# Kernel optimization log

Measured on AMD Instinct MI355X. Metric: run time of the kernel, lower is better.

Reference implementation:

```python
import jax, jax.numpy as jnp
import numpy as np

EPS = 1e-5

def layer_norm(x, g, b):
    mu = jnp.mean(x, axis=-1, keepdims=True)
    var = jnp.mean(jnp.square(x - mu), axis=-1, keepdims=True)
    return (x - mu) * jax.lax.rsqrt(var + EPS) * g + b

def setup_inputs() -> dict:
    key = jax.random.key(0)
    ks = jax.random.split(key, 16)
    B, S, D, H, T = 8, 1024, 512, 8, 6
    Dff = 4 * D
    s = 0.02
    return {
        "x": jax.random.normal(ks[0], (B, S, D), jnp.float32),
        "signal_type_ids": jax.random.randint(ks[1], (B, S), 0, T, jnp.int32),
        "emb": jax.random.normal(ks[2], (T, D), jnp.float32) * s,
        "in_proj_w": jax.random.normal(ks[3], (3 * D, D), jnp.float32) * s,
        "in_proj_b": jnp.zeros((3 * D,), jnp.float32),
        "out_proj_w": jax.random.normal(ks[4], (D, D), jnp.float32) * s,
        "out_proj_b": jnp.zeros((D,), jnp.float32),
        "ln1_g": jnp.ones((D,), jnp.float32),
        "ln1_b": jnp.zeros((D,), jnp.float32),
        "ln2_g": jnp.ones((D,), jnp.float32),
        "ln2_b": jnp.zeros((D,), jnp.float32),
        "w1": jax.random.normal(ks[5], (Dff, D), jnp.float32) * s,
        "b1": jnp.zeros((Dff,), jnp.float32),
        "w2": jax.random.normal(ks[6], (D, Dff), jnp.float32) * s,
        "b2": jnp.zeros((D,), jnp.float32),
    }

def reference(x, signal_type_ids, emb, in_proj_w, in_proj_b, out_proj_w, out_proj_b,
              ln1_g, ln1_b, ln2_g, ln2_b, w1, b1, w2, b2):
    B, S, D = x.shape
    H = 8
    hd = D // H
    # embedding add
    x = x + emb[signal_type_ids]
    # pre-norm MHA (need_weights=True path, average_attn_weights=True)
    xn = layer_norm(x, ln1_g, ln1_b)
    qkv = xn @ in_proj_w.T + in_proj_b            # [B,S,3D]
    q, k, v = jnp.split(qkv, 3, axis=-1)
    q = q.reshape(B, S, H, hd)
    k = k.reshape(B, S, H, hd)
    v = v.reshape(B, S, H, hd)
    scores = jnp.einsum("bqhd,bkhd->bhqk", q, k) / jnp.sqrt(jnp.asarray(hd, x.dtype))
    attn = jax.nn.softmax(scores, axis=-1)        # [B,H,S,S]
    attn_weights = jnp.mean(attn, axis=1)         # averaged over heads [B,S,S]
    ctx = jnp.einsum("bhqk,bkhd->bqhd", attn, v).reshape(B, S, D)
    attn_out = ctx @ out_proj_w.T + out_proj_b
    x = x + attn_out
    # FFN with exact GELU (torch nn.GELU default)
    h = layer_norm(x, ln2_g, ln2_b)
    h = jax.nn.gelu(h @ w1.T + b1, approximate=False)
    x = x + h @ w2.T + b2
    return x, attn_weights
```

## Files before the change

### kernel.cpp

```cpp
#include <hip/hip_runtime.h>
#include <math.h>

constexpr int CB = 8;
constexpr int CS = 1024;
constexpr int CD = 512;
constexpr int CH = 8;
constexpr int CHD = 64;
constexpr int CDFF = 2048;
constexpr int NROW = CB * CS;

typedef unsigned short u16;
typedef unsigned int u32;
typedef __attribute__((ext_vector_type(8))) short short8;
typedef __attribute__((ext_vector_type(8))) unsigned short ushort8v;
typedef __attribute__((ext_vector_type(4))) float floatx4;

__device__ inline u16 f2bf(float f) {
    union { float f; unsigned u; } v; v.f = f;
    unsigned u = v.u + 0x7FFFu + ((v.u >> 16) & 1u);
    return (u16)(u >> 16);
}
__device__ inline float bf2f(u16 h) {
    union { unsigned u; float f; } v; v.u = ((unsigned)h) << 16;
    return v.f;
}

__device__ inline void gload16(const u16* g, u16* l) {
    __builtin_amdgcn_global_load_lds(
        (const __attribute__((address_space(1))) u32*)g,
        (__attribute__((address_space(3))) u32*)l, 16, 0, 0);
}

__global__ __launch_bounds__(256) void ln_kernel(
    const float* __restrict__ x, const int* __restrict__ ids,
    const float* __restrict__ emb,
    const float* __restrict__ g, const float* __restrict__ beta,
    float* __restrict__ xr_out, u16* __restrict__ xn_out)
{
    __shared__ float red1[4], red2[4];
    __shared__ float mu_s, ri_s;
    int row = blockIdx.x;
    int tid = threadIdx.x;
    int d0 = tid * 2;
    const float* xrow = x + (size_t)row * CD;
    float2 xv = *(const float2*)(xrow + d0);
    float v0 = xv.x, v1 = xv.y;
    if (emb) {
        int id = ids[row];
        float2 ev = *(const float2*)(emb + (size_t)id * CD + d0);
        v0 += ev.x; v1 += ev.y;
    }
    float s1 = v0 + v1;
    float s2 = v0 * v0 + v1 * v1;
    for (int off = 32; off > 0; off >>= 1) {
        s1 += __shfl_down(s1, off, 64);
        s2 += __shfl_down(s2, off, 64);
    }
    int wave = tid >> 6;
    if ((tid & 63) == 0) { red1[wave] = s1; red2[wave] = s2; }
    __syncthreads();
    if (tid == 0) {
        float t1 = red1[0] + red1[1] + red1[2] + red1[3];
        float t2 = red2[0] + red2[1] + red2[2] + red2[3];
        float mu = t1 / CD;
        float var = t2 / CD - mu * mu;
        mu_s = mu;
        ri_s = rsqrtf(var + 1e-5f);
    }
    __syncthreads();
    float mu = mu_s, ri = ri_s;
    if (xr_out) {
        float2 o; o.x = v0; o.y = v1;
        *(float2*)(xr_out + (size_t)row * CD + d0) = o;
    }
    float2 gv = *(const float2*)(g + d0);
    float2 bv = *(const float2*)(beta + d0);
    float n0 = (v0 - mu) * ri * gv.x + bv.x;
    float n1 = (v1 - mu) * ri * gv.y + bv.y;
    u32 pk = (u32)f2bf(n0) | ((u32)f2bf(n1) << 16);
    *(u32*)(xn_out + (size_t)row * CD + d0) = pk;
}

__global__ __launch_bounds__(256) void conv_kernel(
    const float* __restrict__ src, u16* __restrict__ dst)
{
    size_t i = ((size_t)blockIdx.x * 256 + threadIdx.x) * 8;
    float4 a = *(const float4*)(src + i);
    float4 b = *(const float4*)(src + i + 4);
    ushort8v o;
    o[0] = f2bf(a.x); o[1] = f2bf(a.y); o[2] = f2bf(a.z); o[3] = f2bf(a.w);
    o[4] = f2bf(b.x); o[5] = f2bf(b.y); o[6] = f2bf(b.z); o[7] = f2bf(b.w);
    *(ushort8v*)(dst + i) = o;
}

template <int ACT, int RES, int OUTBF>
__global__ __launch_bounds__(256) void gemm_mfma(
    const u16* __restrict__ A, const u16* __restrict__ W,
    const float* __restrict__ bias, const float* __restrict__ res,
    void* __restrict__ Cout, int M, int N, int K)
{
    __shared__ u16 As[128 * 32];
    __shared__ u16 Bs[128 * 32];
    int t = threadIdx.x;
    int lane = t & 63;
    int w = t >> 6;
    int m0 = blockIdx.x * 128;
    int n0 = blockIdx.y * 128;
    int col = lane & 15;
    int quad = lane >> 4;
    int wm = w & 1, wn = w >> 1;

    const u16* ag = A + (size_t)(m0 + (t >> 2)) * K + (t & 3) * 8;
    const u16* ag2 = ag + (size_t)64 * K;
    const u16* bg = W + (size_t)(n0 + (t >> 2)) * K + (t & 3) * 8;
    const u16* bg2 = bg + (size_t)64 * K;
    u16* la = As + w * 512;
    u16* lb = Bs + w * 512;

    floatx4 acc[4][4];
#pragma unroll
    for (int i = 0; i < 4; i++)
#pragma unroll
        for (int j = 0; j < 4; j++) acc[i][j] = (floatx4){0.f, 0.f, 0.f, 0.f};

    for (int kt = 0; kt < K; kt += 32) {
        gload16(ag + kt, la);
        gload16(ag2 + kt, la + 2048);
        gload16(bg + kt, lb);
        gload16(bg2 + kt, lb + 2048);
        __syncthreads();
        short8 af[4], bf[4];
#pragma unroll
        for (int mi = 0; mi < 4; mi++)
            af[mi] = *(const short8*)&As[(wm * 64 + mi * 16 + col) * 32 + quad * 8];
#pragma unroll
        for (int ni = 0; ni < 4; ni++)
            bf[ni] = *(const short8*)&Bs[(wn * 64 + ni * 16 + col) * 32 + quad * 8];
#pragma unroll
        for (int mi = 0; mi < 4; mi++)
#pragma unroll
            for (int ni = 0; ni < 4; ni++)
                acc[mi][ni] = __builtin_amdgcn_mfma_f32_16x16x32_bf16(
                    af[mi], bf[ni], acc[mi][ni], 0, 0, 0);
        __syncthreads();
    }

#pragma unroll
    for (int mi = 0; mi < 4; mi++)
#pragma unroll
        for (int ni = 0; ni < 4; ni++) {
            int c = n0 + wn * 64 + ni * 16 + col;
            float bv = bias[c];
#pragma unroll
            for (int r = 0; r < 4; r++) {
                int m = m0 + wm * 64 + mi * 16 + quad * 4 + r;
                float v = acc[mi][ni][r] + bv;
                if (ACT == 1) v = 0.5f * v * (1.0f + erff(v * 0.70710678118654752f));
                if (RES) v += res[(size_t)m * N + c];
                if (OUTBF) ((u16*)Cout)[(size_t)m * N + c] = f2bf(v);
                else       ((float*)Cout)[(size_t)m * N + c] = v;
            }
        }
}

template <int ACT, int RES, int OUTBF>
__global__ __launch_bounds__(256) void gemm_mfma64(
    const u16* __restrict__ A, const u16* __restrict__ W,
    const float* __restrict__ bias, const float* __restrict__ res,
    void* __restrict__ Cout, int M, int N, int K)
{
    __shared__ u16 As[64 * 32];
    __shared__ u16 Bs[128 * 32];
    int t = threadIdx.x;
    int lane = t & 63;
    int w = t >> 6;
    int m0 = blockIdx.x * 64;
    int n0 = blockIdx.y * 128;
    int col = lane & 15;
    int quad = lane >> 4;

    const u16* ag = A + (size_t)(m0 + (t >> 2)) * K + (t & 3) * 8;
    const u16* bg = W + (size_t)(n0 + (t >> 2)) * K + (t & 3) * 8;
    const u16* bg2 = bg + (size_t)64 * K;
    u16* la = As + w * 512;
    u16* lb = Bs + w * 512;

    floatx4 acc[4][2];
#pragma unroll
    for (int i = 0; i < 4; i++)
#pragma unroll
        for (int j = 0; j < 2; j++) acc[i][j] = (floatx4){0.f, 0.f, 0.f, 0.f};

    for (int kt = 0; kt < K; kt += 32) {
        gload16(ag + kt, la);
        gload16(bg + kt, lb);
        gload16(bg2 + kt, lb + 2048);
        __syncthreads();
        short8 af[4], bf[2];
#pragma unroll
        for (int mi = 0; mi < 4; mi++)
            af[mi] = *(const short8*)&As[(mi * 16 + col) * 32 + quad * 8];
#pragma unroll
        for (int ni = 0; ni < 2; ni++)
            bf[ni] = *(const short8*)&Bs[(w * 32 + ni * 16 + col) * 32 + quad * 8];
#pragma unroll
        for (int mi = 0; mi < 4; mi++)
#pragma unroll
            for (int ni = 0; ni < 2; ni++)
                acc[mi][ni] = __builtin_amdgcn_mfma_f32_16x16x32_bf16(
                    af[mi], bf[ni], acc[mi][ni], 0, 0, 0);
        __syncthreads();
    }

#pragma unroll
    for (int mi = 0; mi < 4; mi++)
#pragma unroll
        for (int ni = 0; ni < 2; ni++) {
            int c = n0 + w * 32 + ni * 16 + col;
            float bv = bias[c];
#pragma unroll
            for (int r = 0; r < 4; r++) {
                int m = m0 + mi * 16 + quad * 4 + r;
                float v = acc[mi][ni][r] + bv;
                if (ACT == 1) v = 0.5f * v * (1.0f + erff(v * 0.70710678118654752f));
                if (RES) v += res[(size_t)m * N + c];
                if (OUTBF) ((u16*)Cout)[(size_t)m * N + c] = f2bf(v);
                else       ((float*)Cout)[(size_t)m * N + c] = v;
            }
        }
}

__global__ __launch_bounds__(256) void vt_kernel(
    const u16* __restrict__ qkvb, u16* __restrict__ vt)
{
    __shared__ u16 tile[64][72];
    int b = blockIdx.x >> 4;
    int s0 = (blockIdx.x & 15) * 64;
    int h = blockIdx.y;
    int t = threadIdx.x;
    int r = t >> 2;
    int c0 = (t & 3) * 16;
    const u16* src = qkvb + (size_t)(b * CS + s0 + r) * 1536 + 2 * CD + h * CHD + c0;
    *(ushort8v*)&tile[r][c0] = *(const ushort8v*)src;
    *(ushort8v*)&tile[r][c0 + 8] = *(const ushort8v*)(src + 8);
    __syncthreads();
    u16* dst = vt + (((size_t)b * CH + h) * CHD + r) * CS + s0 + c0;
    ushort8v lo, hi;
#pragma unroll
    for (int j = 0; j < 8; j++) { lo[j] = tile[c0 + j][r]; hi[j] = tile[c0 + 8 + j][r]; }
    *(ushort8v*)dst = lo;
    *(ushort8v*)(dst + 8) = hi;
}

__global__ __launch_bounds__(256, 4) void attn_qk_kernel(
    const u16* __restrict__ qkvb,
    u16* __restrict__ Se, float* __restrict__ Lout, int b0)
{
    __shared__ u16 Qs[2][64 * 32];
    __shared__ u16 Ks[2][2][64 * 32];
    __shared__ float rs[4][4][16];

    int t = threadIdx.x;
    int lane = t & 63;
    int w = t >> 6;
    int col = lane & 15;
    int quad = lane >> 4;
    int bid = blockIdx.x;
    int xcd = bid & 7;
    int j = bid >> 3;
    int bhl = xcd * 4 + (j >> 4);
    int qt = j & 15;
    int lb = bhl >> 3, h = bhl & 7;
    int b = b0 + lb;
    int q0 = qt * 64;
    int bh = b * CH + h;
    size_t splane = (size_t)(lb * CH + h) * CS * CS;

    int srow = t >> 2;
    int scol = (t & 3) * 8;

    {
        const u16* qsrc = qkvb + (size_t)(b * CS + q0 + srow) * 1536 + h * CHD + scol;
        gload16(qsrc, Qs[0] + w * 512);
        gload16(qsrc + 32, Qs[1] + w * 512);
        const u16* ksrc = qkvb + (size_t)(b * CS + srow) * 1536 + CD + h * CHD + scol;
        gload16(ksrc, Ks[0][0] + w * 512);
        gload16(ksrc + 32, Ks[0][1] + w * 512);
    }
    __syncthreads();

    float esum[4] = {0.f, 0.f, 0.f, 0.f};
    for (int kc = 0; kc < 16; kc++) {
        int cur = kc & 1;
        if (kc < 15) {
            const u16* ksrc = qkvb + (size_t)(b * CS + (kc + 1) * 64 + srow) * 1536
                              + CD + h * CHD + scol;
            gload16(ksrc, Ks[cur ^ 1][0] + w * 512);
            gload16(ksrc + 32, Ks[cur ^ 1][1] + w * 512);
        }
        short8 af0 = *(const short8*)&Ks[cur][0][(w * 16 + col) * 32 + quad * 8];
        short8 af1 = *(const short8*)&Ks[cur][1][(w * 16 + col) * 32 + quad * 8];
#pragma unroll
        for (int nq = 0; nq < 4; nq++) {
            short8 bf0 = *(const short8*)&Qs[0][(nq * 16 + col) * 32 + quad * 8];
            short8 bf1 = *(const short8*)&Qs[1][(nq * 16 + col) * 32 + quad * 8];
            floatx4 c = {0.f, 0.f, 0.f, 0.f};
            c = __builtin_amdgcn_mfma_f32_16x16x32_bf16(af0, bf0, c, 0, 0, 0);
            c = __builtin_amdgcn_mfma_f32_16x16x32_bf16(af1, bf1, c, 0, 0, 0);
            float e0 = __expf(c[0] * 0.125f);
            float e1 = __expf(c[1] * 0.125f);
            float e2 = __expf(c[2] * 0.125f);
            float e3 = __expf(c[3] * 0.125f);
            esum[nq] += (e0 + e1) + (e2 + e3);
            union { float f; u32 u; } a0, a1, a2, a3;
            a0.f = e0; a1.f = e1; a2.f = e2; a3.f = e3;
            u32* sp = (u32*)(Se + splane + (size_t)(q0 + nq * 16 + col) * CS
                             + kc * 64 + w * 16 + quad * 4);
            sp[0] = (a0.u >> 16) | (a1.u & 0xFFFF0000u);
            sp[1] = (a2.u >> 16) | (a3.u & 0xFFFF0000u);
        }
        __syncthreads();
    }

#pragma unroll
    for (int nq = 0; nq < 4; nq++) {
        float v = esum[nq];
        v += __shfl_xor(v, 16, 64);
        v += __shfl_xor(v, 32, 64);
        if (quad == 0) rs[w][nq][col] = v;
    }
    __syncthreads();
    if (t < 64) {
        int nq = t >> 4, c2 = t & 15;
        float L = rs[0][nq][c2] + rs[1][nq][c2] + rs[2][nq][c2] + rs[3][nq][c2];
        Lout[((size_t)bh << 10) + q0 + nq * 16 + c2] = L;
    }
}

__global__ __launch_bounds__(256, 4) void attn_pv_kernel(
    const u16* __restrict__ Se, const u16* __restrict__ vt,
    const float* __restrict__ Lin, u16* __restrict__ ctx, int b0)
{
    __shared__ u16 Ss[2][2][64 * 32];
    __shared__ u16 Vs[2][2][64 * 32];

    int t = threadIdx.x;
    int lane = t & 63;
    int w = t >> 6;
    int col = lane & 15;
    int quad = lane >> 4;
    int bid = blockIdx.x;
    int xcd = bid & 7;
    int j = bid >> 3;
    int bhl = xcd * 4 + (j >> 4);
    int qt = j & 15;
    int lb = bhl >> 3, h = bhl & 7;
    int b = b0 + lb;
    int q0 = qt * 64;
    int bh = b * CH + h;
    size_t splane = (size_t)(lb * CH + h) * CS * CS;

    int srow = t >> 2;
    int scol = (t & 3) * 8;

    const u16* sbase = Se + splane + (size_t)(q0 + srow) * CS + scol;
    const u16* vbase = vt + ((size_t)bh * CHD + srow) * CS + scol;

    gload16(sbase, Ss[0][0] + w * 512);
    gload16(sbase + 32, Ss[0][1] + w * 512);
    gload16(vbase, Vs[0][0] + w * 512);
    gload16(vbase + 32, Vs[0][1] + w * 512);
    __syncthreads();

    floatx4 acc[4];
#pragma unroll
    for (int i = 0; i < 4; i++) acc[i] = (floatx4){0.f, 0.f, 0.f, 0.f};

    for (int kc = 0; kc < 16; kc++) {
        int cur = kc & 1;
        if (kc < 15) {
            int ko = (kc + 1) * 64;
            gload16(sbase + ko, Ss[cur ^ 1][0] + w * 512);
            gload16(sbase + ko + 32, Ss[cur ^ 1][1] + w * 512);
            gload16(vbase + ko, Vs[cur ^ 1][0] + w * 512);
            gload16(vbase + ko + 32, Vs[cur ^ 1][1] + w * 512);
        }
        short8 af0 = *(const short8*)&Ss[cur][0][(w * 16 + col) * 32 + quad * 8];
        short8 af1 = *(const short8*)&Ss[cur][1][(w * 16 + col) * 32 + quad * 8];
#pragma unroll
        for (int nd = 0; nd < 4; nd++) {
            short8 bf0 = *(const short8*)&Vs[cur][0][(nd * 16 + col) * 32 + quad * 8];
            short8 bf1 = *(const short8*)&Vs[cur][1][(nd * 16 + col) * 32 + quad * 8];
            acc[nd] = __builtin_amdgcn_mfma_f32_16x16x32_bf16(af0, bf0, acc[nd], 0, 0, 0);
            acc[nd] = __builtin_amdgcn_mfma_f32_16x16x32_bf16(af1, bf1, acc[nd], 0, 0, 0);
        }
        __syncthreads();
    }

    int qg = q0 + w * 16 + quad * 4;
    float li[4];
#pragma unroll
    for (int r = 0; r < 4; r++)
        li[r] = 1.0f / Lin[((size_t)bh << 10) + qg + r];
    u16* cb = ctx + ((size_t)(b * CS) + qg) * CD + h * CHD + col;
#pragma unroll
    for (int nd = 0; nd < 4; nd++)
#pragma unroll
        for (int r = 0; r < 4; r++)
            cb[(size_t)r * CD + nd * 16] = f2bf(acc[nd][r] * li[r]);
}

__global__ __launch_bounds__(256, 8) void attn_aw_kernel(
    const u16* __restrict__ Se, const float* __restrict__ Lin,
    float* __restrict__ aw_out, int b0)
{
    int bq = blockIdx.x;
    int bl = bq >> 9;
    int b = b0 + bl;
    int q = (bq & 511) * 2 + (threadIdx.x >> 7);
    int k0 = (threadIdx.x & 127) * 8;

    float acc[8];
#pragma unroll
    for (int i = 0; i < 8; i++) acc[i] = 0.f;

#pragma unroll
    for (int h = 0; h < CH; h++) {
        float linv = 0.125f / Lin[(((size_t)(b * CH + h)) << 10) + q];
        const u16* sp = Se + ((size_t)(bl * CH + h) * CS + q) * CS + k0;
        ushort8v e = *(const ushort8v*)sp;
#pragma unroll
        for (int i = 0; i < 8; i++) acc[i] += bf2f(e[i]) * linv;
    }
    float* ap = aw_out + ((size_t)(b * CS) + q) * CS + k0;
    *(float4*)ap = make_float4(acc[0], acc[1], acc[2], acc[3]);
    *(float4*)(ap + 4) = make_float4(acc[4], acc[5], acc[6], acc[7]);
}

extern "C" void kernel_launch(void* const* d_in, const int* in_sizes, int n_in,
                              void* d_out, int out_size, void* d_ws, size_t ws_size,
                              hipStream_t stream)
{
    const float* x    = (const float*)d_in[0];
    const int*   ids  = (const int*)d_in[1];
    const float* emb  = (const float*)d_in[2];
    const float* inw  = (const float*)d_in[3];
    const float* inb  = (const float*)d_in[4];
    const float* ow   = (const float*)d_in[5];
    const float* ob   = (const float*)d_in[6];
    const float* g1   = (const float*)d_in[7];
    const float* be1  = (const float*)d_in[8];
    const float* g2   = (const float*)d_in[9];
    const float* be2  = (const float*)d_in[10];
    const float* w1   = (const float*)d_in[11];
    const float* b1   = (const float*)d_in[12];
    const float* w2   = (const float*)d_in[13];
    const float* b2   = (const float*)d_in[14];

    float* out_x  = (float*)d_out;
    float* out_aw = out_x + (size_t)CB * CS * CD;

    char* p = (char*)d_ws;
    float* xr   = (float*)p; p += (size_t)NROW * CD * 4;
    float* x2   = (float*)p; p += (size_t)NROW * CD * 4;
    u16* xnb    = (u16*)p;   p += (size_t)NROW * CD * 2;
    u16* qkvb   = (u16*)p;   p += (size_t)NROW * 3 * CD * 2;
    u16* ctxb   = (u16*)p;   p += (size_t)NROW * CD * 2;
    u16* hidb   = (u16*)p;   p += (size_t)NROW * CDFF * 2;
    u16* inwb   = (u16*)p;   p += (size_t)3 * CD * CD * 2;
    u16* owb    = (u16*)p;   p += (size_t)CD * CD * 2;
    u16* w1b    = (u16*)p;   p += (size_t)CDFF * CD * 2;
    u16* w2b    = (u16*)p;   p += (size_t)CD * CDFF * 2;
    float* Lbuf = (float*)p; p += (size_t)CB * CH * CS * 4;
    u16* Se     = (u16*)p;   p += (size_t)(CB / 2) * CH * CS * CS * 2;

    u16* vtb = hidb;

    dim3 blk(256);
    conv_kernel<<<(3 * CD * CD) / 2048, blk, 0, stream>>>(inw, inwb);
    conv_kernel<<<(CD * CD) / 2048, blk, 0, stream>>>(ow, owb);
    conv_kernel<<<(CDFF * CD) / 2048, blk, 0, stream>>>(w1, w1b);
    conv_kernel<<<(CD * CDFF) / 2048, blk, 0, stream>>>(w2, w2b);
    ln_kernel<<<NROW, blk, 0, stream>>>(x, ids, emb, g1, be1, xr, xnb);
    gemm_mfma<0, 0, 1><<<dim3(NROW / 128, (3 * CD) / 128), blk, 0, stream>>>(
        xnb, inwb, inb, nullptr, qkvb, NROW, 3 * CD, CD);
    vt_kernel<<<dim3(CB * (CS / 64), CH), blk, 0, stream>>>(qkvb, vtb);
    for (int half = 0; half < 2; half++) {
        int b0 = half * 4;
        attn_qk_kernel<<<512, blk, 0, stream>>>(qkvb, Se, Lbuf, b0);
        attn_pv_kernel<<<512, blk, 0, stream>>>(Se, vtb, Lbuf, ctxb, b0);
        attn_aw_kernel<<<2048, blk, 0, stream>>>(Se, Lbuf, out_aw, b0);
    }
    gemm_mfma64<0, 1, 0><<<dim3(NROW / 64, CD / 128), blk, 0, stream>>>(
        ctxb, owb, ob, xr, x2, NROW, CD, CD);
    ln_kernel<<<NROW, blk, 0, stream>>>(x2, nullptr, nullptr, g2, be2, nullptr, xnb);
    gemm_mfma<1, 0, 1><<<dim3(NROW / 128, CDFF / 128), blk, 0, stream>>>(
        xnb, w1b, b1, nullptr, hidb, NROW, CDFF, CD);
    gemm_mfma64<0, 1, 0><<<dim3(NROW / 64, CD / 128), blk, 0, stream>>>(
        hidb, w2b, b2, x2, out_x, NROW, CD, CDFF);
}
```

Measured before the change: 357.8 us.

## Fuse attention QK-exp and PV kernels, keep scores in LDS for PV

Merges the QK/exp kernel and the PV kernel into one attention kernel. Each 64-key chunk's exponentiated scores go into an LDS tile and are consumed by the PV MFMAs right away, so the bf16 score plane is no longer read back from global memory for PV. It is still written out for the averaged-attention kernel. Q fragments are hoisted into registers, and the normalizer comes from the block's own row sums rather than a global reload. The four weight-conversion launches are also merged into one kernel, at the cost of more LDS, lower occupancy (launch bounds 256,2) and an extra barrier per chunk.

```diff
diff --git a/kernel.cpp b/kernel.cpp
--- a/kernel.cpp
+++ b/kernel.cpp
@@ -81,12 +81,20 @@
     *(u32*)(xn_out + (size_t)row * CD + d0) = pk;
 }
 
-__global__ __launch_bounds__(256) void conv_kernel(
-    const float* __restrict__ src, u16* __restrict__ dst)
+__global__ __launch_bounds__(256) void conv4_kernel(
+    const float* __restrict__ s0, const float* __restrict__ s1,
+    const float* __restrict__ s2, const float* __restrict__ s3,
+    u16* __restrict__ dst)
 {
     size_t i = ((size_t)blockIdx.x * 256 + threadIdx.x) * 8;
-    float4 a = *(const float4*)(src + i);
-    float4 b = *(const float4*)(src + i + 4);
+    const float* src;
+    size_t off;
+    if (i < 786432)        { src = s0; off = i; }
+    else if (i < 1048576)  { src = s1; off = i - 786432; }
+    else if (i < 2097152)  { src = s2; off = i - 1048576; }
+    else                   { src = s3; off = i - 2097152; }
+    float4 a = *(const float4*)(src + off);
+    float4 b = *(const float4*)(src + off + 4);
     ushort8v o;
     o[0] = f2bf(a.x); o[1] = f2bf(a.y); o[2] = f2bf(a.z); o[3] = f2bf(a.w);
     o[4] = f2bf(b.x); o[5] = f2bf(b.y); o[6] = f2bf(b.z); o[7] = f2bf(b.w);
@@ -252,12 +260,15 @@
     *(ushort8v*)(dst + 8) = hi;
 }
 
-__global__ __launch_bounds__(256, 4) void attn_qk_kernel(
-    const u16* __restrict__ qkvb,
-    u16* __restrict__ Se, float* __restrict__ Lout, int b0)
+__global__ __launch_bounds__(256, 2) void attn_fused_kernel(
+    const u16* __restrict__ qkvb, const u16* __restrict__ vt,
+    u16* __restrict__ Se, float* __restrict__ Lout,
+    u16* __restrict__ ctx, int b0)
 {
     __shared__ u16 Qs[2][64 * 32];
     __shared__ u16 Ks[2][2][64 * 32];
+    __shared__ u16 Vs[2][2][64 * 32];
+    __shared__ u16 S[64][72];
     __shared__ float rs[4][4][16];
 
     int t = threadIdx.x;
@@ -279,34 +290,41 @@
     int srow = t >> 2;
     int scol = (t & 3) * 8;
 
+    const u16* ksrc0 = qkvb + (size_t)(b * CS + srow) * 1536 + CD + h * CHD + scol;
+    const u16* vsrc0 = vt + ((size_t)bh * CHD + srow) * CS + scol;
+
     {
         const u16* qsrc = qkvb + (size_t)(b * CS + q0 + srow) * 1536 + h * CHD + scol;
         gload16(qsrc, Qs[0] + w * 512);
         gload16(qsrc + 32, Qs[1] + w * 512);
-        const u16* ksrc = qkvb + (size_t)(b * CS + srow) * 1536 + CD + h * CHD + scol;
-        gload16(ksrc, Ks[0][0] + w * 512);
-        gload16(ksrc + 32, Ks[0][1] + w * 512);
+        gload16(ksrc0, Ks[0][0] + w * 512);
+        gload16(ksrc0 + 32, Ks[0][1] + w * 512);
+        gload16(vsrc0, Vs[0][0] + w * 512);
+        gload16(vsrc0 + 32, Vs[0][1] + w * 512);
     }
     __syncthreads();
 
+    short8 qf[2][4];
+#pragma unroll
+    for (int dsl = 0; dsl < 2; dsl++)
+#pragma unroll
+        for (int nq = 0; nq < 4; nq++)
+            qf[dsl][nq] = *(const short8*)&Qs[dsl][(nq * 16 + col) * 32 + quad * 8];
+
+    floatx4 acc[4];
+#pragma unroll
+    for (int i = 0; i < 4; i++) acc[i] = (floatx4){0.f, 0.f, 0.f, 0.f};
     float esum[4] = {0.f, 0.f, 0.f, 0.f};
+
     for (int kc = 0; kc < 16; kc++) {
         int cur = kc & 1;
-        if (kc < 15) {
-            const u16* ksrc = qkvb + (size_t)(b * CS + (kc + 1) * 64 + srow) * 1536
-                              + CD + h * CHD + scol;
-            gload16(ksrc, Ks[cur ^ 1][0] + w * 512);
-            gload16(ksrc + 32, Ks[cur ^ 1][1] + w * 512);
-        }
-        short8 af0 = *(const short8*)&Ks[cur][0][(w * 16 + col) * 32 + quad * 8];
-        short8 af1 = *(const short8*)&Ks[cur][1][(w * 16 + col) * 32 + quad * 8];
+        short8 kf0 = *(const short8*)&Ks[cur][0][(w * 16 + col) * 32 + quad * 8];
+        short8 kf1 = *(const short8*)&Ks[cur][1][(w * 16 + col) * 32 + quad * 8];
 #pragma unroll
         for (int nq = 0; nq < 4; nq++) {
-            short8 bf0 = *(const short8*)&Qs[0][(nq * 16 + col) * 32 + quad * 8];
-            short8 bf1 = *(const short8*)&Qs[1][(nq * 16 + col) * 32 + quad * 8];
             floatx4 c = {0.f, 0.f, 0.f, 0.f};
-            c = __builtin_amdgcn_mfma_f32_16x16x32_bf16(af0, bf0, c, 0, 0, 0);
-            c = __builtin_amdgcn_mfma_f32_16x16x32_bf16(af1, bf1, c, 0, 0, 0);
+            c = __builtin_amdgcn_mfma_f32_16x16x32_bf16(kf0, qf[0][nq], c, 0, 0, 0);
+            c = __builtin_amdgcn_mfma_f32_16x16x32_bf16(kf1, qf[1][nq], c, 0, 0, 0);
             float e0 = __expf(c[0] * 0.125f);
             float e1 = __expf(c[1] * 0.125f);
             float e2 = __expf(c[2] * 0.125f);
@@ -314,10 +332,33 @@
             esum[nq] += (e0 + e1) + (e2 + e3);
             union { float f; u32 u; } a0, a1, a2, a3;
             a0.f = e0; a1.f = e1; a2.f = e2; a3.f = e3;
-            u32* sp = (u32*)(Se + splane + (size_t)(q0 + nq * 16 + col) * CS
+            u32 p0 = (a0.u >> 16) | (a1.u & 0xFFFF0000u);
+            u32 p1 = (a2.u >> 16) | (a3.u & 0xFFFF0000u);
+            u32* sp = (u32*)&S[nq * 16 + col][w * 16 + quad * 4];
+            sp[0] = p0; sp[1] = p1;
+            u32* gp = (u32*)(Se + splane + (size_t)(q0 + nq * 16 + col) * CS
                              + kc * 64 + w * 16 + quad * 4);
-            sp[0] = (a0.u >> 16) | (a1.u & 0xFFFF0000u);
-            sp[1] = (a2.u >> 16) | (a3.u & 0xFFFF0000u);
+            gp[0] = p0; gp[1] = p1;
+        }
+        __syncthreads();
+
+        if (kc < 15) {
+            int ko = (kc + 1) * 64;
+            const u16* ks = ksrc0 + (size_t)ko * 1536;
+            gload16(ks, Ks[cur ^ 1][0] + w * 512);
+            gload16(ks + 32, Ks[cur ^ 1][1] + w * 512);
+            gload16(vsrc0 + ko, Vs[cur ^ 1][0] + w * 512);
+            gload16(vsrc0 + ko + 32, Vs[cur ^ 1][1] + w * 512);
+        }
+
+        short8 sf0 = *(const short8*)&S[w * 16 + col][quad * 8];
+        short8 sf1 = *(const short8*)&S[w * 16 + col][32 + quad * 8];
+#pragma unroll
+        for (int nd = 0; nd < 4; nd++) {
+            short8 vf0 = *(const short8*)&Vs[cur][0][(nd * 16 + col) * 32 + quad * 8];
+            short8 vf1 = *(const short8*)&Vs[cur][1][(nd * 16 + col) * 32 + quad * 8];
+            acc[nd] = __builtin_amdgcn_mfma_f32_16x16x32_bf16(sf0, vf0, acc[nd], 0, 0, 0);
+            acc[nd] = __builtin_amdgcn_mfma_f32_16x16x32_bf16(sf1, vf1, acc[nd], 0, 0, 0);
         }
         __syncthreads();
     }
@@ -335,74 +376,14 @@
         float L = rs[0][nq][c2] + rs[1][nq][c2] + rs[2][nq][c2] + rs[3][nq][c2];
         Lout[((size_t)bh << 10) + q0 + nq * 16 + c2] = L;
     }
-}
-
-__global__ __launch_bounds__(256, 4) void attn_pv_kernel(
-    const u16* __restrict__ Se, const u16* __restrict__ vt,
-    const float* __restrict__ Lin, u16* __restrict__ ctx, int b0)
-{
-    __shared__ u16 Ss[2][2][64 * 32];
-    __shared__ u16 Vs[2][2][64 * 32];
-
-    int t = threadIdx.x;
-    int lane = t & 63;
-    int w = t >> 6;
-    int col = lane & 15;
-    int quad = lane >> 4;
-    int bid = blockIdx.x;
-    int xcd = bid & 7;
-    int j = bid >> 3;
-    int bhl = xcd * 4 + (j >> 4);
-    int qt = j & 15;
-    int lb = bhl >> 3, h = bhl & 7;
-    int b = b0 + lb;
-    int q0 = qt * 64;
-    int bh = b * CH + h;
-    size_t splane = (size_t)(lb * CH + h) * CS * CS;
-
-    int srow = t >> 2;
-    int scol = (t & 3) * 8;
-
-    const u16* sbase = Se + splane + (size_t)(q0 + srow) * CS + scol;
-    const u16* vbase = vt + ((size_t)bh * CHD + srow) * CS + scol;
-
-    gload16(sbase, Ss[0][0] + w * 512);
-    gload16(sbase + 32, Ss[0][1] + w * 512);
-    gload16(vbase, Vs[0][0] + w * 512);
-    gload16(vbase + 32, Vs[0][1] + w * 512);
-    __syncthreads();
-
-    floatx4 acc[4];
-#pragma unroll
-    for (int i = 0; i < 4; i++) acc[i] = (floatx4){0.f, 0.f, 0.f, 0.f};
-
-    for (int kc = 0; kc < 16; kc++) {
-        int cur = kc & 1;
-        if (kc < 15) {
-            int ko = (kc + 1) * 64;
-            gload16(sbase + ko, Ss[cur ^ 1][0] + w * 512);
-            gload16(sbase + ko + 32, Ss[cur ^ 1][1] + w * 512);
-            gload16(vbase + ko, Vs[cur ^ 1][0] + w * 512);
-            gload16(vbase + ko + 32, Vs[cur ^ 1][1] + w * 512);
-        }
-        short8 af0 = *(const short8*)&Ss[cur][0][(w * 16 + col) * 32 + quad * 8];
-        short8 af1 = *(const short8*)&Ss[cur][1][(w * 16 + col) * 32 + quad * 8];
-#pragma unroll
-        for (int nd = 0; nd < 4; nd++) {
-            short8 bf0 = *(const short8*)&Vs[cur][0][(nd * 16 + col) * 32 + quad * 8];
-            short8 bf1 = *(const short8*)&Vs[cur][1][(nd * 16 + col) * 32 + quad * 8];
-            acc[nd] = __builtin_amdgcn_mfma_f32_16x16x32_bf16(af0, bf0, acc[nd], 0, 0, 0);
-            acc[nd] = __builtin_amdgcn_mfma_f32_16x16x32_bf16(af1, bf1, acc[nd], 0, 0, 0);
-        }
-        __syncthreads();
-    }
-
-    int qg = q0 + w * 16 + quad * 4;
+
     float li[4];
 #pragma unroll
-    for (int r = 0; r < 4; r++)
-        li[r] = 1.0f / Lin[((size_t)bh << 10) + qg + r];
-    u16* cb = ctx + ((size_t)(b * CS) + qg) * CD + h * CHD + col;
+    for (int r = 0; r < 4; r++) {
+        int cr = quad * 4 + r;
+        li[r] = 1.0f / (rs[0][w][cr] + rs[1][w][cr] + rs[2][w][cr] + rs[3][w][cr]);
+    }
+    u16* cb = ctx + ((size_t)(b * CS) + q0 + w * 16 + quad * 4) * CD + h * CHD + col;
 #pragma unroll
     for (int nd = 0; nd < 4; nd++)
 #pragma unroll
@@ -477,18 +458,15 @@
     u16* vtb = hidb;
 
     dim3 blk(256);
-    conv_kernel<<<(3 * CD * CD) / 2048, blk, 0, stream>>>(inw, inwb);
-    conv_kernel<<<(CD * CD) / 2048, blk, 0, stream>>>(ow, owb);
-    conv_kernel<<<(CDFF * CD) / 2048, blk, 0, stream>>>(w1, w1b);
-    conv_kernel<<<(CD * CDFF) / 2048, blk, 0, stream>>>(w2, w2b);
+    conv4_kernel<<<(3 * CD * CD + CD * CD + 2 * CDFF * CD) / 2048, blk, 0, stream>>>(
+        inw, ow, w1, w2, inwb);
     ln_kernel<<<NROW, blk, 0, stream>>>(x, ids, emb, g1, be1, xr, xnb);
     gemm_mfma<0, 0, 1><<<dim3(NROW / 128, (3 * CD) / 128), blk, 0, stream>>>(
         xnb, inwb, inb, nullptr, qkvb, NROW, 3 * CD, CD);
     vt_kernel<<<dim3(CB * (CS / 64), CH), blk, 0, stream>>>(qkvb, vtb);
     for (int half = 0; half < 2; half++) {
         int b0 = half * 4;
-        attn_qk_kernel<<<512, blk, 0, stream>>>(qkvb, Se, Lbuf, b0);
-        attn_pv_kernel<<<512, blk, 0, stream>>>(Se, vtb, Lbuf, ctxb, b0);
+        attn_fused_kernel<<<512, blk, 0, stream>>>(qkvb, vtb, Se, Lbuf, ctxb, b0);
         attn_aw_kernel<<<2048, blk, 0, stream>>>(Se, Lbuf, out_aw, b0);
     }
     gemm_mfma64<0, 1, 0><<<dim3(NROW / 64, CD / 128), blk, 0, stream>>>(
```

After: 325.1 us. 1.1x faster.
